# Kernel optimization log

Hardware: AMD Instinct MI355X
Metric: run time of the kernel (lower is better)

Reference implementation:

```python
import jax, jax.numpy as jnp
import numpy as np

B, T, I, H = 4, 128, 32, 64


def setup_inputs() -> dict:
    key = jax.random.key(0)
    k1, k2, k3 = jax.random.split(key, 3)
    x = jax.random.normal(k1, (B, T, I), dtype=jnp.float32)
    carry = jnp.zeros((B, H), dtype=jnp.float32)  # RNNCell.initialize_carry uses zeros
    # lecun_normal-like input kernel (default_kernel_init)
    Wi = jax.random.normal(k2, (I, H), dtype=jnp.float32) / np.float32(np.sqrt(I))
    # orthogonal recurrent kernel init
    Wh, _ = jnp.linalg.qr(jax.random.normal(k3, (H, H), dtype=jnp.float32))
    b = jnp.zeros((H,), dtype=jnp.float32)
    return {"carry": carry, "x": x, "Wi": Wi, "Wh": Wh, "b": b}


def reference(carry, x, Wi, Wh, b):
    # Vanilla RNN step: a = tanh(x_t @ Wi + h @ Wh + b), scanned over time (axis 1).
    # Per step we also emit the analytic forward-mode Jacobian of the new state
    # w.r.t. (Wi, Wh, b, carry) -- exactly what jacfwd(fn, argnums=(0,1)) computes.
    Hh = Wh.shape[0]
    Bb = carry.shape[0]
    eyeH = jnp.eye(Hh, dtype=x.dtype)
    eyeB = jnp.eye(Bb, dtype=x.dtype)

    def step(h, x_t):
        a = jnp.tanh(x_t @ Wi + h @ Wh + b)  # (B, H)
        g = 1.0 - a * a                      # tanh' at preactivation, (B, H)
        # d a[b,j] / d Wi[i,k] = g[b,j] * x[b,i] * delta(j,k)  -> (B, H, I, H)
        J_Wi = jnp.einsum('bj,bi,jk->bjik', g, x_t, eyeH)
        # d a[b,j] / d Wh[m,k] = g[b,j] * h[b,m] * delta(j,k)  -> (B, H, H, H)
        J_Wh = jnp.einsum('bj,bm,jk->bjmk', g, h, eyeH)
        # d a[b,j] / d b[k]    = g[b,j] * delta(j,k)           -> (B, H, H)
        J_b = jnp.einsum('bj,jk->bjk', g, eyeH)
        # d a[b,j] / d h[c,m]  = g[b,j] * Wh[m,j] * delta(b,c) -> (B, H, B, H)
        J_h = jnp.einsum('bj,mj,bc->bjcm', g, Wh, eyeB)
        return a, (a, J_Wi, J_Wh, J_b, J_h)

    final_carry, ys = jax.lax.scan(step, carry, jnp.moveaxis(x, 1, 0))
    # out_axes=1: time axis goes to position 1 of every output leaf
    out, J_Wi, J_Wh, J_b, J_h = jax.tree.map(lambda y: jnp.moveaxis(y, 0, 1), ys)
    return final_carry, out, J_Wi, J_Wh, J_b, J_h
```

## Files before the change

kernel.cpp:

```cpp
#include <hip/hip_runtime.h>
#include <math.h>

#define OFF_OUT   256u
#define OFF_JWI   33024u
#define OFF_JWH   67141888u
#define OFF_JB    201359616u
#define OFF_JH    203456768u
#define OUT_TOTAL 211845376u

#define JWI4 8256u
#define JWH4 16785472u
#define JB4  50339904u
#define JH4  50864192u
#define END4 52961344u

typedef float f32x4 __attribute__((ext_vector_type(4)));

static __device__ __forceinline__ float tanh_fast(float x) {
    float t = __expf(2.0f * x);
    return 1.0f - 2.0f / (t + 1.0f);
}

__global__ __launch_bounds__(256) void whT_kernel(
    const float* __restrict__ Wh, float* __restrict__ whT)
{
    const int p = blockIdx.x * 256 + threadIdx.x;
    const int m = p >> 6, k = p & 63;
    whT[k * 64 + m] = Wh[p];
}

__global__ __launch_bounds__(256) void xwi_kernel(
    const float* __restrict__ x, const float* __restrict__ Wi,
    const float* __restrict__ bias, float* __restrict__ out)
{
    const int tid = threadIdx.x;
    const int row = blockIdx.x * 4 + (tid >> 6);
    const int j = tid & 63;
    const float* xr = x + row * 32;
    float acc = bias[j];
#pragma unroll
    for (int i = 0; i < 32; ++i) acc = fmaf(xr[i], Wi[i * 64 + j], acc);
    out[OFF_OUT + row * 64 + j] = acc;
}

__global__ __launch_bounds__(64) void scan_kernel(
    const float* __restrict__ carry, const float* __restrict__ Wh,
    float* __restrict__ out, float* __restrict__ hprev)
{
    const int b = blockIdx.x;
    const int j = threadIdx.x;
    float wcol[64];
#pragma unroll
    for (int m = 0; m < 64; ++m) wcol[m] = Wh[m * 64 + j];

    __shared__ __align__(16) float sh[64];
    float a_prev = carry[b * 64 + j];
    sh[j] = a_prev;
    float* ub = out + OFF_OUT + b * 8192;
    float* hb = hprev + b * 8192;
    float u0 = ub[j];
    float u1 = ub[64 + j];
    const f32x4* shv = reinterpret_cast<const f32x4*>(sh);
    float a = 0.0f;

    for (int t = 0; t < 128; ++t) {
        hb[t * 64 + j] = a_prev;
        const float pre = u0;
        u0 = u1;
        if (t + 2 < 128) u1 = ub[(t + 2) * 64 + j];
        float s0 = 0.f, s1 = 0.f, s2 = 0.f, s3 = 0.f;
#pragma unroll
        for (int mm = 0; mm < 16; ++mm) {
            const f32x4 hv = shv[mm];
            s0 = fmaf(hv.x, wcol[mm * 4 + 0], s0);
            s1 = fmaf(hv.y, wcol[mm * 4 + 1], s1);
            s2 = fmaf(hv.z, wcol[mm * 4 + 2], s2);
            s3 = fmaf(hv.w, wcol[mm * 4 + 3], s3);
        }
        a = tanh_fast(pre + (s0 + s1) + (s2 + s3));
        ub[t * 64 + j] = a;
        sh[j] = a;
        a_prev = a;
    }
    out[b * 64 + j] = a;
}

__global__ __launch_bounds__(256) void fill_sweep(
    const float* __restrict__ x, float* __restrict__ out,
    const float* __restrict__ whT, const float* __restrict__ hprev)
{
    const float* __restrict__ outh = out + OFF_OUT;
    const f32x4* __restrict__ whT4 = reinterpret_cast<const f32x4*>(whT);
    f32x4* __restrict__ o4 = reinterpret_cast<f32x4*>(out);
    const unsigned stride = gridDim.x * blockDim.x;

#pragma unroll 2
    for (unsigned v = JWI4 + blockIdx.x * blockDim.x + threadIdx.x;
         v < END4; v += stride) {
        f32x4 r;
        if (v < JWH4) {
            const unsigned u = v - JWI4;
            const unsigned k4 = u & 15u;
            const unsigned row = u >> 4;
            const unsigned i = row & 31u;
            const unsigned jj = (row >> 5) & 63u;
            const unsigned bt = row >> 11;
            const float a = outh[bt * 64u + jj];
            const float val = (1.0f - a * a) * x[bt * 32u + i];
            const unsigned d = jj - k4 * 4u;
            r.x = (d == 0u) ? val : 0.f; r.y = (d == 1u) ? val : 0.f;
            r.z = (d == 2u) ? val : 0.f; r.w = (d == 3u) ? val : 0.f;
        } else if (v < JB4) {
            const unsigned u = v - JWH4;
            const unsigned k4 = u & 15u;
            const unsigned row = u >> 4;
            const unsigned m = row & 63u;
            const unsigned jj = (row >> 6) & 63u;
            const unsigned bt = row >> 12;
            const float a = outh[bt * 64u + jj];
            const float val = (1.0f - a * a) * hprev[bt * 64u + m];
            const unsigned d = jj - k4 * 4u;
            r.x = (d == 0u) ? val : 0.f; r.y = (d == 1u) ? val : 0.f;
            r.z = (d == 2u) ? val : 0.f; r.w = (d == 3u) ? val : 0.f;
        } else if (v < JH4) {
            const unsigned u = v - JB4;
            const unsigned k4 = u & 15u;
            const unsigned row = u >> 4;
            const unsigned jj = row & 63u;
            const float a = outh[row];
            const float g = 1.0f - a * a;
            const unsigned d = jj - k4 * 4u;
            r.x = (d == 0u) ? g : 0.f; r.y = (d == 1u) ? g : 0.f;
            r.z = (d == 2u) ? g : 0.f; r.w = (d == 3u) ? g : 0.f;
        } else {
            const unsigned u = v - JH4;
            const unsigned k4 = u & 15u;
            const unsigned row = u >> 4;
            const unsigned c = row & 3u;
            const unsigned jj = (row >> 2) & 63u;
            const unsigned bt = row >> 8;
            const unsigned b = bt >> 7;
            const float a = outh[bt * 64u + jj];
            const float g = 1.0f - a * a;
            const f32x4 w4 = whT4[jj * 16u + k4];
            const bool on = (c == b);
            r.x = on ? g * w4.x : 0.f; r.y = on ? g * w4.y : 0.f;
            r.z = on ? g * w4.z : 0.f; r.w = on ? g * w4.w : 0.f;
        }
        __builtin_nontemporal_store(r, o4 + v);
    }
}

extern "C" void kernel_launch(void* const* d_in, const int* in_sizes, int n_in,
                              void* d_out, int out_size, void* d_ws, size_t ws_size,
                              hipStream_t stream) {
    const float* carry = (const float*)d_in[0];
    const float* x     = (const float*)d_in[1];
    const float* Wi    = (const float*)d_in[2];
    const float* Wh    = (const float*)d_in[3];
    const float* bias  = (const float*)d_in[4];
    float* out = (float*)d_out;
    float* whT   = (float*)d_ws;
    float* hprev = whT + 4096;

    whT_kernel <<<16, 256, 0, stream>>>(Wh, whT);
    xwi_kernel <<<128, 256, 0, stream>>>(x, Wi, bias, out);
    scan_kernel<<<4, 64, 0, stream>>>(carry, Wh, out, hprev);
    fill_sweep <<<2048, 256, 0, stream>>>(x, out, whT, hprev);
}
```

Measured before the change: 215.7 us.

## Replace grid-stride Jacobian fill with per-block zero-then-scatter tiles

Replaces the grid-stride sweep, which computes every float4 of the Jacobian outputs, with one 256 KB tile per block. Each block first writes zeros over its whole tile with vector stores, then scatters only the non-zero diagonal or block-diagonal entries after a barrier. This removes the per-element index decoding and branching and drops the Wh-transpose kernel by reading Wh directly. The cost is extra writes to the nonzero positions, a loss of nontemporal stores, and a dependence on write ordering within a block.

New measurement: 295.3 us. +36.9%, slower.

```diff
diff --git a/kernel.cpp b/kernel.cpp
--- a/kernel.cpp
+++ b/kernel.cpp
@@ -6,27 +6,12 @@
 #define OFF_JWH   67141888u
 #define OFF_JB    201359616u
 #define OFF_JH    203456768u
-#define OUT_TOTAL 211845376u
-
-#define JWI4 8256u
-#define JWH4 16785472u
-#define JB4  50339904u
-#define JH4  50864192u
-#define END4 52961344u
 
 typedef float f32x4 __attribute__((ext_vector_type(4)));
 
 static __device__ __forceinline__ float tanh_fast(float x) {
     float t = __expf(2.0f * x);
     return 1.0f - 2.0f / (t + 1.0f);
-}
-
-__global__ __launch_bounds__(256) void whT_kernel(
-    const float* __restrict__ Wh, float* __restrict__ whT)
-{
-    const int p = blockIdx.x * 256 + threadIdx.x;
-    const int m = p >> 6, k = p & 63;
-    whT[k * 64 + m] = Wh[p];
 }
 
 __global__ __launch_bounds__(256) void xwi_kernel(
@@ -85,69 +70,85 @@
     out[b * 64 + j] = a;
 }
 
-__global__ __launch_bounds__(256) void fill_sweep(
-    const float* __restrict__ x, float* __restrict__ out,
-    const float* __restrict__ whT, const float* __restrict__ hprev)
+__global__ __launch_bounds__(256) void fill_kernel(
+    const float* __restrict__ x, const float* __restrict__ Wh,
+    float* __restrict__ out, const float* __restrict__ hprev)
 {
+    const int tid = threadIdx.x;
+    const unsigned blk = blockIdx.x;
     const float* __restrict__ outh = out + OFF_OUT;
-    const f32x4* __restrict__ whT4 = reinterpret_cast<const f32x4*>(whT);
-    f32x4* __restrict__ o4 = reinterpret_cast<f32x4*>(out);
-    const unsigned stride = gridDim.x * blockDim.x;
 
-#pragma unroll 2
-    for (unsigned v = JWI4 + blockIdx.x * blockDim.x + threadIdx.x;
-         v < END4; v += stride) {
-        f32x4 r;
-        if (v < JWH4) {
-            const unsigned u = v - JWI4;
-            const unsigned k4 = u & 15u;
-            const unsigned row = u >> 4;
-            const unsigned i = row & 31u;
-            const unsigned jj = (row >> 5) & 63u;
-            const unsigned bt = row >> 11;
-            const float a = outh[bt * 64u + jj];
-            const float val = (1.0f - a * a) * x[bt * 32u + i];
-            const unsigned d = jj - k4 * 4u;
-            r.x = (d == 0u) ? val : 0.f; r.y = (d == 1u) ? val : 0.f;
-            r.z = (d == 2u) ? val : 0.f; r.w = (d == 3u) ? val : 0.f;
-        } else if (v < JB4) {
-            const unsigned u = v - JWH4;
-            const unsigned k4 = u & 15u;
-            const unsigned row = u >> 4;
-            const unsigned m = row & 63u;
-            const unsigned jj = (row >> 6) & 63u;
-            const unsigned bt = row >> 12;
-            const float a = outh[bt * 64u + jj];
-            const float val = (1.0f - a * a) * hprev[bt * 64u + m];
-            const unsigned d = jj - k4 * 4u;
-            r.x = (d == 0u) ? val : 0.f; r.y = (d == 1u) ? val : 0.f;
-            r.z = (d == 2u) ? val : 0.f; r.w = (d == 3u) ? val : 0.f;
-        } else if (v < JH4) {
-            const unsigned u = v - JB4;
-            const unsigned k4 = u & 15u;
-            const unsigned row = u >> 4;
-            const unsigned jj = row & 63u;
-            const float a = outh[row];
+    size_t base;
+    if (blk < 2048u)      base = OFF_JWH + (size_t)blk * 65536u;
+    else if (blk < 3072u) base = OFF_JWI + (size_t)(blk - 2048u) * 65536u;
+    else if (blk < 3104u) base = OFF_JB  + (size_t)(blk - 3072u) * 65536u;
+    else                  base = OFF_JH  + (size_t)(blk - 3104u) * 65536u;
+
+    f32x4* s4 = reinterpret_cast<f32x4*>(out + base);
+    const f32x4 z = {0.f, 0.f, 0.f, 0.f};
+#pragma unroll 4
+    for (int k = 0; k < 64; ++k)
+        s4[k * 256 + tid] = z;
+    __syncthreads();
+
+    if (blk < 2048u) {
+        const unsigned bt = blk >> 2, jq = blk & 3u;
+        const float* hb = hprev + bt * 64u;
+#pragma unroll
+        for (int k = 0; k < 4; ++k) {
+            const unsigned p = tid + k * 256u;
+            const unsigned jl = p >> 6, m = p & 63u;
+            const unsigned jg = jq * 16u + jl;
+            const float a = outh[bt * 64u + jg];
+            const float v = (1.0f - a * a) * hb[m];
+            const unsigned d = jg & 3u;
+            f32x4 r = { d == 0u ? v : 0.f, d == 1u ? v : 0.f,
+                        d == 2u ? v : 0.f, d == 3u ? v : 0.f };
+            *reinterpret_cast<f32x4*>(out + base + (size_t)p * 64u + (jg & ~3u)) = r;
+        }
+    } else if (blk < 3072u) {
+        const unsigned idx = blk - 2048u;
+        const unsigned bt = idx >> 1, jh = idx & 1u;
+#pragma unroll
+        for (int k = 0; k < 4; ++k) {
+            const unsigned p = tid + k * 256u;
+            const unsigned jl = p >> 5, i = p & 31u;
+            const unsigned jg = jh * 32u + jl;
+            const float a = outh[bt * 64u + jg];
+            const float v = (1.0f - a * a) * x[bt * 32u + i];
+            const unsigned d = jg & 3u;
+            f32x4 r = { d == 0u ? v : 0.f, d == 1u ? v : 0.f,
+                        d == 2u ? v : 0.f, d == 3u ? v : 0.f };
+            *reinterpret_cast<f32x4*>(out + base + (size_t)p * 64u + (jg & ~3u)) = r;
+        }
+    } else if (blk < 3104u) {
+        const unsigned c = blk - 3072u;
+#pragma unroll
+        for (int k = 0; k < 4; ++k) {
+            const unsigned pl = tid + k * 256u;
+            const unsigned j = pl & 63u;
+            const float a = outh[c * 1024u + pl];
             const float g = 1.0f - a * a;
-            const unsigned d = jj - k4 * 4u;
-            r.x = (d == 0u) ? g : 0.f; r.y = (d == 1u) ? g : 0.f;
-            r.z = (d == 2u) ? g : 0.f; r.w = (d == 3u) ? g : 0.f;
-        } else {
-            const unsigned u = v - JH4;
-            const unsigned k4 = u & 15u;
-            const unsigned row = u >> 4;
-            const unsigned c = row & 3u;
-            const unsigned jj = (row >> 2) & 63u;
-            const unsigned bt = row >> 8;
-            const unsigned b = bt >> 7;
-            const float a = outh[bt * 64u + jj];
+            const unsigned d = j & 3u;
+            f32x4 r = { d == 0u ? g : 0.f, d == 1u ? g : 0.f,
+                        d == 2u ? g : 0.f, d == 3u ? g : 0.f };
+            *reinterpret_cast<f32x4*>(out + base + (size_t)pl * 64u + (j & ~3u)) = r;
+        }
+    } else {
+        const unsigned q = blk - 3104u;
+        const unsigned b = (q * 4u) >> 7;
+        const unsigned m0 = (tid & 15u) * 4u;
+#pragma unroll 4
+        for (int k = 0; k < 16; ++k) {
+            const unsigned rr = (tid >> 4) + k * 16u;
+            const unsigned s = rr >> 6, j = rr & 63u;
+            const float a = outh[(q * 4u + s) * 64u + j];
             const float g = 1.0f - a * a;
-            const f32x4 w4 = whT4[jj * 16u + k4];
-            const bool on = (c == b);
-            r.x = on ? g * w4.x : 0.f; r.y = on ? g * w4.y : 0.f;
-            r.z = on ? g * w4.z : 0.f; r.w = on ? g * w4.w : 0.f;
+            f32x4 r = { g * Wh[(m0 + 0u) * 64u + j], g * Wh[(m0 + 1u) * 64u + j],
+                        g * Wh[(m0 + 2u) * 64u + j], g * Wh[(m0 + 3u) * 64u + j] };
+            *reinterpret_cast<f32x4*>(
+                out + base + ((size_t)rr * 4u + b) * 64u + m0) = r;
         }
-        __builtin_nontemporal_store(r, o4 + v);
     }
 }
 
@@ -160,11 +161,9 @@
     const float* Wh    = (const float*)d_in[3];
     const float* bias  = (const float*)d_in[4];
     float* out = (float*)d_out;
-    float* whT   = (float*)d_ws;
-    float* hprev = whT + 4096;
+    float* hprev = (float*)d_ws;
 
-    whT_kernel <<<16, 256, 0, stream>>>(Wh, whT);
     xwi_kernel <<<128, 256, 0, stream>>>(x, Wi, bias, out);
     scan_kernel<<<4, 64, 0, stream>>>(carry, Wh, out, hprev);
-    fill_sweep <<<2048, 256, 0, stream>>>(x, out, whT, hprev);
+    fill_kernel<<<3232, 256, 0, stream>>>(x, Wh, out, hprev);
 }
```
